# Optimization experiments

Measured on AMD Instinct MI355X. Metric: run time of the kernel, lower is better.

## Reference

```python
import jax, jax.numpy as jnp
import numpy as np

NEG_INF = -1e9

def setup_inputs() -> dict:
    key = jax.random.key(0)
    ks = jax.random.split(key, 7)
    B, NQ, NK, DQ, DK, DV, DH = 16, 128, 2048, 256, 256, 128, 64
    queries = jax.random.normal(ks[0], (B, NQ, DQ), dtype=jnp.float32)
    keys = jax.random.normal(ks[1], (B, NK, DK), dtype=jnp.float32)
    values = jax.random.normal(ks[2], (B, NK, DV), dtype=jnp.float32)
    valid_lens = jax.random.randint(ks[3], (B,), 1, NK + 1, dtype=jnp.int32)
    Wq = jax.random.normal(ks[4], (DQ, DH), dtype=jnp.float32) / np.sqrt(DQ)
    Wk = jax.random.normal(ks[5], (DK, DH), dtype=jnp.float32) / np.sqrt(DK)
    wv = jax.random.normal(ks[6], (DH,), dtype=jnp.float32) / np.sqrt(DH)
    return {"queries": queries, "keys": keys, "values": values,
            "valid_lens": valid_lens, "Wq": Wq, "Wk": Wk, "wv": wv}


def reference(queries, keys, values, valid_lens, Wq, Wk, wv):
    # Additive (Bahdanau) attention.
    q = jnp.einsum('bqd,dh->bqh', queries, Wq)   # [B, nq, dH]
    k = jnp.einsum('bkd,dh->bkh', keys, Wk)      # [B, nk, dH]
    # broadcast add -> tanh -> reduce with wv: scores [B, nq, nk]
    feat = jnp.tanh(q[:, :, None, :] + k[:, None, :, :])  # [B, nq, nk, dH]
    scores = jnp.einsum('bqkh,h->bqk', feat, wv)
    # masked softmax over nk using per-batch valid lengths
    nk = keys.shape[1]
    mask = jnp.arange(nk)[None, None, :] < valid_lens[:, None, None]  # [B,1,nk]
    scores = jnp.where(mask, scores, NEG_INF)
    attn = jax.nn.softmax(scores, axis=-1)
    # dropout is identity at eval time
    return jnp.einsum('bqk,bkv->bqv', attn, values)  # [B, nq, dv]
```

## Files before the change

kernel.cpp:

```cpp
#include <hip/hip_runtime.h>
#include <stddef.h>


__device__ __forceinline__ float fast_rcp(float x)  { return __builtin_amdgcn_rcpf(x); }
__device__ __forceinline__ float fast_exp2(float x) { return __builtin_amdgcn_exp2f(x); }

#define C2F 2.88539008177792681f
#define L2E 1.44269504088896340f

#define M_CNTP 0
#define M_CNTS 1
#define M_NP   2
#define M_NS   3
#define M_PPK  8
#define M_PSC  32

__global__ void init_kernel(const int* __restrict__ vlens, int* __restrict__ meta)
{
  if (threadIdx.x == 0) {
    int ap = 0, as = 0;
    meta[M_PPK] = 0; meta[M_PSC] = 0;
    for (int b = 0; b < 16; ++b) {
      int vl = vlens[b];
      ap += (vl + 63) >> 6;
      as += (vl + 127) >> 7;
      meta[M_PPK + 1 + b] = ap;
      meta[M_PSC + 1 + b] = as;
    }
    meta[M_NP]   = 32 + ap;
    meta[M_NS]   = as * 8;
    meta[M_CNTP] = 0;
    meta[M_CNTS] = 0;
  }
}

template<int MODE>
__device__ __forceinline__
void proj_body(const float* __restrict__ inb, const float* __restrict__ W,
               float* __restrict__ out, int b, int r0, int rowsPerB, int t)
{
  __shared__ float4 Wlds[256 * 16];
  __shared__ float  klds[64 * 36];

  const float4* W4 = (const float4*)W;
  #pragma unroll
  for (int i = 0; i < 16; ++i) Wlds[t + 256 * i] = W4[t + 256 * i];

  const int j = t >> 4;
  const int g = t & 15;

  float acc[4][4];
  #pragma unroll
  for (int m = 0; m < 4; ++m)
    acc[m][0] = acc[m][1] = acc[m][2] = acc[m][3] = 0.f;

  for (int dc = 0; dc < 8; ++dc) {
    {
      const int row = t >> 2, cs = (t & 3) * 8;
      const float* s = inb + row * 256 + dc * 32 + cs;
      float4 a0 = *(const float4*)s;
      float4 a1 = *(const float4*)(s + 4);
      float* dst = &klds[row * 36 + cs];
      *(float4*)dst       = a0;
      *(float4*)(dst + 4) = a1;
    }
    __syncthreads();
    #pragma unroll
    for (int d = 0; d < 32; ++d) {
      float4 w4 = Wlds[(dc * 32 + d) * 16 + j];
      #pragma unroll
      for (int m = 0; m < 4; ++m) {
        float kv = klds[(g + 16 * m) * 36 + d];
        acc[m][0] = fmaf(kv, w4.x, acc[m][0]);
        acc[m][1] = fmaf(kv, w4.y, acc[m][1]);
        acc[m][2] = fmaf(kv, w4.z, acc[m][2]);
        acc[m][3] = fmaf(kv, w4.w, acc[m][3]);
      }
    }
    __syncthreads();
  }

  if constexpr (MODE == 1) {
    #pragma unroll
    for (int m = 0; m < 4; ++m) {
      int k = r0 + g + 16 * m;
      size_t base = ((size_t)(b * 16 + (k >> 7)) * 64) * 128 + (k & 127);
      #pragma unroll
      for (int i = 0; i < 4; ++i)
        out[base + (size_t)(4 * j + i) * 128] = fast_exp2(C2F * acc[m][i]);
    }
  } else if constexpr (MODE == 2) {
    #pragma unroll
    for (int m = 0; m < 4; ++m) {
      int k = r0 + g + 16 * m;
      size_t base = (size_t)(b * 16 + (k >> 7)) * 8192 + (size_t)(k & 127) * 2;
      float e0 = fast_exp2(C2F * acc[m][0]);
      float e1 = fast_exp2(C2F * acc[m][1]);
      float e2 = fast_exp2(C2F * acc[m][2]);
      float e3 = fast_exp2(C2F * acc[m][3]);
      *(float2*)&out[base + (size_t)(2 * j) * 256]     = make_float2(e0, e1);
      *(float2*)&out[base + (size_t)(2 * j + 1) * 256] = make_float2(e2, e3);
    }
  } else {
    #pragma unroll
    for (int m = 0; m < 4; ++m) {
      int row = r0 + g + 16 * m;
      float4 o;
      o.x = fast_exp2(C2F * acc[m][0]);
      o.y = fast_exp2(C2F * acc[m][1]);
      o.z = fast_exp2(C2F * acc[m][2]);
      o.w = fast_exp2(C2F * acc[m][3]);
      *(float4*)&out[((size_t)b * rowsPerB + row) * 64 + 4 * j] = o;
    }
  }
}

__global__ __launch_bounds__(256)
void proj_qk_kernel(const float* __restrict__ queries, const float* __restrict__ keys,
                    const float* __restrict__ Wq, const float* __restrict__ Wk,
                    float* __restrict__ Eq, float* __restrict__ EkP,
                    int* __restrict__ meta)
{
  __shared__ int sh_u;
  const int t = threadIdx.x;
  const int nunits = meta[M_NP];
  for (;;) {
    __syncthreads();
    if (t == 0) sh_u = atomicAdd(&meta[M_CNTP], 1);
    __syncthreads();
    const int u = sh_u;
    if (u >= nunits) break;
    if (u < 32) {
      const int b = u & 15, rt = u >> 4, r0 = rt * 64;
      proj_body<0>(queries + ((size_t)b * 128 + r0) * 256, Wq, Eq, b, r0, 128, t);
    } else {
      int w = u - 32;
      int b = 0;
      while (w >= meta[M_PPK + 1 + b]) ++b;
      const int rt = w - meta[M_PPK + b];
      const int r0 = rt * 64;
      proj_body<2>(keys + ((size_t)b * 2048 + r0) * 256, Wk, EkP, b, r0, 2048, t);
    }
  }
}

template<int MODE, bool CHECK>
__global__ __launch_bounds__(256)
void proj_kernel(const float* __restrict__ in, const float* __restrict__ W,
                 float* __restrict__ out, const int* __restrict__ vlens,
                 int rowsPerB)
{
  const int t  = threadIdx.x;
  const int b  = blockIdx.x & 15;
  const int rt = blockIdx.x >> 4;
  const int r0 = rt * 64;
  if constexpr (CHECK) {
    if (r0 >= vlens[b]) return;
  }
  proj_body<MODE>(in + ((size_t)b * rowsPerB + r0) * 256, W, out, b, r0,
                  rowsPerB, t);
}

__global__ __launch_bounds__(512, 8)
void scorepv_kernel(const float* __restrict__ Eq, const float* __restrict__ EkP,
                    const float* __restrict__ values, const int* __restrict__ vlens,
                    const float* __restrict__ wv,
                    float* __restrict__ partial, float* __restrict__ tsum,
                    int* __restrict__ meta)
{
  __shared__ float ek_lds[64 * 128];
  __shared__ int sh_u;

  const int t = threadIdx.x;
  const int nunits = meta[M_NS];

  float w0 = 0.f, W1 = 0.f;
  #pragma unroll
  for (int u = 0; u < 16; ++u) {
    float4 v = ((const float4*)wv)[u];
    w0 += v.x + v.y + v.z + v.w;
    W1 += fabsf(v.x) + fabsf(v.y) + fabsf(v.z) + fabsf(v.w);
  }

  for (;;) {
    __syncthreads();
    if (t == 0) sh_u = atomicAdd(&meta[M_CNTS], 1);
    __syncthreads();
    const int u = sh_u;
    if (u >= nunits) break;

    const int w  = u >> 3;
    const int qq = u & 7;
    int b = 0;
    while (w >= meta[M_PSC + 1 + b]) ++b;
    const int kt = w - meta[M_PSC + b];
    const int vl = vlens[b];

    {
      const float4* src = (const float4*)(EkP + (size_t)(b * 16 + kt) * 8192);
      float4* dst = (float4*)ek_lds;
      #pragma unroll
      for (int i = 0; i < 4; ++i) dst[t + 512 * i] = src[t + 512 * i];
    }
    __syncthreads();

    const int wave_u = __builtin_amdgcn_readfirstlane(t >> 6);
    const int lane   = t & 63;
    const int q0g    = qq * 16 + wave_u * 2;
    const int kp     = lane * 2;
    const float* eqb = Eq + (size_t)(b * 128 + q0g) * 64;

    float s[2][2] = {{w0, w0}, {w0, w0}};

    const float4* ek4 = (const float4*)ek_lds;
    #pragma unroll 8
    for (int hp = 0; hp < 32; ++hp) {
      float4 e = ek4[hp * 64 + lane];
      float2 wvp = *(const float2*)&wv[2 * hp];
      float wa = -2.0f * wvp.x, wb = -2.0f * wvp.y;
      #pragma unroll
      for (int q = 0; q < 2; ++q) {
        float2 eqp = *(const float2*)&eqb[q * 64 + 2 * hp];
        { float x0 = fmaf(eqp.x, e.x, 1.f), x1 = fmaf(eqp.y, e.y, 1.f);
          float y = fast_rcp(x0 * x1);
          float a = wb * x0; a = fmaf(wa, x1, a);
          s[q][0] = fmaf(a, y, s[q][0]); }
        { float x0 = fmaf(eqp.x, e.z, 1.f), x1 = fmaf(eqp.y, e.w, 1.f);
          float y = fast_rcp(x0 * x1);
          float a = wb * x0; a = fmaf(wa, x1, a);
          s[q][1] = fmaf(a, y, s[q][1]); }
      }
    }

    const int kbase = kt * 128 + kp;
    float p[2][2];
    #pragma unroll
    for (int q = 0; q < 2; ++q) {
      p[q][0] = (kbase     < vl) ? fast_exp2((s[q][0] - W1) * L2E) : 0.f;
      p[q][1] = (kbase + 1 < vl) ? fast_exp2((s[q][1] - W1) * L2E) : 0.f;
    }

    #pragma unroll
    for (int q = 0; q < 2; ++q) {
      float e = p[q][0] + p[q][1];
      #pragma unroll
      for (int m = 1; m < 64; m <<= 1) e += __shfl_xor(e, m, 64);
      if (lane == 0) tsum[(size_t)(b * 16 + kt) * 128 + q0g + q] = e;
    }

    __syncthreads();
    float* p_lds = ek_lds;
    const int q0l = wave_u * 2;
    *(float2*)&p_lds[kp * 20 + q0l]       = make_float2(p[0][0], p[1][0]);
    *(float2*)&p_lds[(kp + 1) * 20 + q0l] = make_float2(p[0][1], p[1][1]);
    __syncthreads();

    const int kg = t >> 7, v = t & 127;
    const int kloc = min(128, vl - kt * 128);
    const int k0 = kg * 32, k1 = min(k0 + 32, kloc);
    const int len = (k1 > k0) ? (k1 - k0) : 0;
    const int nfull = len & ~7;
    const float* vb = values + ((size_t)(b * 2048 + kt * 128)) * 128 + v;
    float acc[16];
    #pragma unroll
    for (int i = 0; i < 16; ++i) acc[i] = 0.f;

    for (int kb = k0; kb < k0 + nfull; kb += 8) {
      float vv[8];
      #pragma unroll
      for (int j = 0; j < 8; ++j) vv[j] = vb[(size_t)(kb + j) * 128];
      #pragma unroll
      for (int j = 0; j < 8; ++j) {
        const float* pr = &p_lds[(kb + j) * 20];
        float4 p0 = *(const float4*)&pr[0];
        float4 p1 = *(const float4*)&pr[4];
        float4 p2 = *(const float4*)&pr[8];
        float4 p3 = *(const float4*)&pr[12];
        float vx = vv[j];
        acc[ 0]=fmaf(p0.x,vx,acc[ 0]); acc[ 1]=fmaf(p0.y,vx,acc[ 1]);
        acc[ 2]=fmaf(p0.z,vx,acc[ 2]); acc[ 3]=fmaf(p0.w,vx,acc[ 3]);
        acc[ 4]=fmaf(p1.x,vx,acc[ 4]); acc[ 5]=fmaf(p1.y,vx,acc[ 5]);
        acc[ 6]=fmaf(p1.z,vx,acc[ 6]); acc[ 7]=fmaf(p1.w,vx,acc[ 7]);
        acc[ 8]=fmaf(p2.x,vx,acc[ 8]); acc[ 9]=fmaf(p2.y,vx,acc[ 9]);
        acc[10]=fmaf(p2.z,vx,acc[10]); acc[11]=fmaf(p2.w,vx,acc[11]);
        acc[12]=fmaf(p3.x,vx,acc[12]); acc[13]=fmaf(p3.y,vx,acc[13]);
        acc[14]=fmaf(p3.z,vx,acc[14]); acc[15]=fmaf(p3.w,vx,acc[15]);
      }
    }
    for (int k = k0 + nfull; k < k1; ++k) {
      float vx = vb[(size_t)k * 128];
      const float* pr = &p_lds[k * 20];
      #pragma unroll
      for (int q = 0; q < 16; ++q) acc[q] = fmaf(pr[q], vx, acc[q]);
    }

    __syncthreads();
    float* red = ek_lds;
    if (kg > 0) {
      #pragma unroll
      for (int q = 0; q < 16; ++q) red[(kg - 1) * 2048 + q * 128 + v] = acc[q];
    }
    __syncthreads();
    if (kg == 0) {
      #pragma unroll
      for (int q = 0; q < 16; ++q) {
        float tot = acc[q] + red[q * 128 + v] + red[2048 + q * 128 + v]
                  + red[4096 + q * 128 + v];
        partial[(((size_t)(b * 128 + qq * 16 + q)) * 16 + kt) * 128 + v] = tot;
      }
    }
  }
}

__global__ __launch_bounds__(256)
void reduce_kernel(const float* __restrict__ partial, const float* __restrict__ tsum,
                   const int* __restrict__ vlens, float* __restrict__ out)
{
  const int blk = blockIdx.x;
  const int b   = blk >> 6;
  const int q   = (blk & 63) * 2 + (threadIdx.x >> 7);
  const int v   = threadIdx.x & 127;
  const int ntk = (vlens[b] + 127) >> 7;

  float tot = 0.f;
  for (int i = 0; i < ntk; ++i)
    tot += tsum[(size_t)(b * 16 + i) * 128 + q];

  float acc = 0.f;
  const float* pp = partial + ((size_t)(b * 128 + q)) * 16 * 128 + v;
  for (int i = 0; i < ntk; ++i)
    acc += pp[(size_t)i * 128];

  out[((size_t)(b * 128 + q)) * 128 + v] = acc / tot;
}

__global__ __launch_bounds__(256)
void attn_kernel(const float* __restrict__ Eq, const float* __restrict__ EkT,
                 const float* __restrict__ values, const int* __restrict__ vlens,
                 const float* __restrict__ wv, float* __restrict__ out)
{
  const int t    = threadIdx.x;
  const int b    = blockIdx.x & 15;
  const int qt   = blockIdx.x >> 4;
  const int wave = t >> 6;
  const int lane = t & 63;

  __shared__ float4 sc4[512 * 4];
  __shared__ float  pvp[128 * 5];
  __shared__ float  linvs[4];

  const int vl = vlens[b];

  float eqv[64], wv2[64];
  float w0 = 0.f;
  {
    const float4* eq4 = (const float4*)(Eq + (size_t)(b * 128 + qt * 4 + wave) * 64);
    const float4* wv4 = (const float4*)wv;
    #pragma unroll
    for (int u = 0; u < 16; ++u) {
      float4 e = eq4[u], v = wv4[u];
      eqv[4*u+0] = e.x; eqv[4*u+1] = e.y; eqv[4*u+2] = e.z; eqv[4*u+3] = e.w;
      wv2[4*u+0] = -2.f * v.x; wv2[4*u+1] = -2.f * v.y;
      wv2[4*u+2] = -2.f * v.z; wv2[4*u+3] = -2.f * v.w;
      w0 += v.x + v.y + v.z + v.w;
    }
  }

  const int ktiles = (vl + 127) >> 7;
  const int kp = 2 * lane;
  for (int kt = 0; kt < ktiles; ++kt) {
    const float* tb = EkT + ((size_t)(b * 16 + kt) * 64) * 128 + kp;
    float s0 = w0, s1 = w0;
    #pragma unroll
    for (int h = 0; h < 64; ++h) {
      float2 ek = *(const float2*)(tb + (size_t)h * 128);
      float r0 = fast_rcp(fmaf(eqv[h], ek.x, 1.0f));
      float r1 = fast_rcp(fmaf(eqv[h], ek.y, 1.0f));
      s0 = fmaf(wv2[h], r0, s0);
      s1 = fmaf(wv2[h], r1, s1);
    }
    int k = kt * 128 + kp;
    if (k     >= vl) s0 = -1e9f;
    if (k + 1 >= vl) s1 = -1e9f;
    float* scf = (float*)sc4;
    *(float2*)(scf + (((k >> 2) * 4 + wave) * 4 + (k & 3))) = make_float2(s0, s1);
  }

  const int nq4 = (vl + 3) >> 2;
  float mx = -3e38f;
  for (int Q = lane; Q < nq4; Q += 64) {
    float4 f = sc4[Q * 4 + wave];
    mx = fmaxf(mx, fmaxf(fmaxf(f.x, f.y), fmaxf(f.z, f.w)));
  }
  #pragma unroll
  for (int msk = 1; msk < 64; msk <<= 1) mx = fmaxf(mx, __shfl_xor(mx, msk, 64));
  float lsum = 0.f;
  for (int Q = lane; Q < nq4; Q += 64) {
    float4 f = sc4[Q * 4 + wave];
    f.x = fast_exp2((f.x - mx) * L2E);
    f.y = fast_exp2((f.y - mx) * L2E);
    f.z = fast_exp2((f.z - mx) * L2E);
    f.w = fast_exp2((f.w - mx) * L2E);
    sc4[Q * 4 + wave] = f;
    lsum += f.x + f.y + f.z + f.w;
  }
  #pragma unroll
  for (int msk = 1; msk < 64; msk <<= 1) lsum += __shfl_xor(lsum, msk, 64);
  if (lane == 0) linvs[wave] = fast_rcp(lsum);
  __syncthreads();

  const int grp = t >> 7, v = t & 127;
  float acc[4] = {0.f, 0.f, 0.f, 0.f};
  const float* vb = values + (size_t)b * 2048 * 128 + v;
  for (int Q = grp; Q < nq4; Q += 2) {
    float4 p0 = sc4[Q * 4 + 0], p1 = sc4[Q * 4 + 1];
    float4 p2 = sc4[Q * 4 + 2], p3 = sc4[Q * 4 + 3];
    const float* vk = vb + (size_t)(Q * 4) * 128;
    float x;
    x = vk[0];
    acc[0]=fmaf(p0.x,x,acc[0]); acc[1]=fmaf(p1.x,x,acc[1]);
    acc[2]=fmaf(p2.x,x,acc[2]); acc[3]=fmaf(p3.x,x,acc[3]);
    x = vk[128];
    acc[0]=fmaf(p0.y,x,acc[0]); acc[1]=fmaf(p1.y,x,acc[1]);
    acc[2]=fmaf(p2.y,x,acc[2]); acc[3]=fmaf(p3.y,x,acc[3]);
    x = vk[256];
    acc[0]=fmaf(p0.z,x,acc[0]); acc[1]=fmaf(p1.z,x,acc[1]);
    acc[2]=fmaf(p2.z,x,acc[2]); acc[3]=fmaf(p3.z,x,acc[3]);
    x = vk[384];
    acc[0]=fmaf(p0.w,x,acc[0]); acc[1]=fmaf(p1.w,x,acc[1]);
    acc[2]=fmaf(p2.w,x,acc[2]); acc[3]=fmaf(p3.w,x,acc[3]);
  }
  if (grp == 1) {
    #pragma unroll
    for (int qq = 0; qq < 4; ++qq) pvp[v * 5 + qq] = acc[qq];
  }
  __syncthreads();
  if (grp == 0) {
    #pragma unroll
    for (int qq = 0; qq < 4; ++qq) {
      float tot = acc[qq] + pvp[v * 5 + qq];
      out[((size_t)(b * 128) + qt * 4 + qq) * 128 + v] = tot * linvs[qq];
    }
  }
}

extern "C" void kernel_launch(void* const* d_in, const int* in_sizes, int n_in,
                              void* d_out, int out_size, void* d_ws, size_t ws_size,
                              hipStream_t stream) {
  const float* queries = (const float*)d_in[0];
  const float* keys    = (const float*)d_in[1];
  const float* values  = (const float*)d_in[2];
  const int*   vlens   = (const int*)d_in[3];
  const float* Wq      = (const float*)d_in[4];
  const float* Wk      = (const float*)d_in[5];
  const float* wv      = (const float*)d_in[6];
  float* outp = (float*)d_out;

  float* base    = (float*)d_ws;
  float* Eq      = base;
  float* EkP     = base + 131072;
  float* tsumb   = base + 2228224;
  float* partial = base + 2260992;
  int*   meta    = (int*)(base + 6455296);
  const size_t need = (size_t)6455296 * 4 + 64 * 4;

  if (ws_size >= need) {
    hipLaunchKernelGGL(init_kernel, dim3(1), dim3(64), 0, stream, vlens, meta);
    hipLaunchKernelGGL(proj_qk_kernel, dim3(512), dim3(256), 0, stream,
                       queries, keys, Wq, Wk, Eq, EkP, meta);
    hipLaunchKernelGGL(scorepv_kernel, dim3(1024), dim3(512), 0, stream,
                       Eq, EkP, values, vlens, wv, partial, tsumb, meta);
    hipLaunchKernelGGL(reduce_kernel, dim3(1024), dim3(256), 0, stream,
                       partial, tsumb, vlens, outp);
  } else {
    hipLaunchKernelGGL((proj_kernel<0, false>), dim3(32), dim3(256), 0, stream,
                       queries, Wq, Eq, (const int*)nullptr, 128);
    hipLaunchKernelGGL((proj_kernel<1, true>), dim3(512), dim3(256), 0, stream,
                       keys, Wk, EkP, vlens, 2048);
    hipLaunchKernelGGL(attn_kernel, dim3(512), dim3(256), 0, stream,
                       Eq, EkP, values, vlens, wv, outp);
  }
}
```

Before: 90.32 us.

## Split fused score/PV kernel and load both projection weights once per block

The fused score+PV kernel becomes two persistent kernels: score_kernel writes per-unit probabilities to a global scratch buffer, and pv_kernel reads them back to do the values matmul. Each kernel can then use its own LDS footprint and occupancy, and the LDS reuse syncs between phases go away. The projection kernel now uses 512-thread blocks that load Wq and Wk into LDS once and keep them across all work units, and prefix tables are cached in shared memory. The cost is an extra global round trip for the probabilities (about 16 MB of scratch), one more launch, and 128 KB of LDS per projection block, which limits how many blocks fit.

```diff
diff --git a/kernel.cpp b/kernel.cpp
--- a/kernel.cpp
+++ b/kernel.cpp
@@ -10,8 +10,9 @@
 
 #define M_CNTP 0
 #define M_CNTS 1
-#define M_NP   2
-#define M_NS   3
+#define M_CNT2 2
+#define M_NP   3
+#define M_NS   4
 #define M_PPK  8
 #define M_PSC  32
 
@@ -31,147 +32,121 @@
     meta[M_NS]   = as * 8;
     meta[M_CNTP] = 0;
     meta[M_CNTS] = 0;
-  }
-}
-
-template<int MODE>
-__device__ __forceinline__
-void proj_body(const float* __restrict__ inb, const float* __restrict__ W,
-               float* __restrict__ out, int b, int r0, int rowsPerB, int t)
-{
-  __shared__ float4 Wlds[256 * 16];
-  __shared__ float  klds[64 * 36];
-
-  const float4* W4 = (const float4*)W;
-  #pragma unroll
-  for (int i = 0; i < 16; ++i) Wlds[t + 256 * i] = W4[t + 256 * i];
-
-  const int j = t >> 4;
-  const int g = t & 15;
-
-  float acc[4][4];
-  #pragma unroll
-  for (int m = 0; m < 4; ++m)
-    acc[m][0] = acc[m][1] = acc[m][2] = acc[m][3] = 0.f;
-
-  for (int dc = 0; dc < 8; ++dc) {
-    {
-      const int row = t >> 2, cs = (t & 3) * 8;
-      const float* s = inb + row * 256 + dc * 32 + cs;
-      float4 a0 = *(const float4*)s;
-      float4 a1 = *(const float4*)(s + 4);
-      float* dst = &klds[row * 36 + cs];
-      *(float4*)dst       = a0;
-      *(float4*)(dst + 4) = a1;
-    }
-    __syncthreads();
-    #pragma unroll
-    for (int d = 0; d < 32; ++d) {
-      float4 w4 = Wlds[(dc * 32 + d) * 16 + j];
-      #pragma unroll
-      for (int m = 0; m < 4; ++m) {
-        float kv = klds[(g + 16 * m) * 36 + d];
-        acc[m][0] = fmaf(kv, w4.x, acc[m][0]);
-        acc[m][1] = fmaf(kv, w4.y, acc[m][1]);
-        acc[m][2] = fmaf(kv, w4.z, acc[m][2]);
-        acc[m][3] = fmaf(kv, w4.w, acc[m][3]);
-      }
-    }
-    __syncthreads();
-  }
-
-  if constexpr (MODE == 1) {
-    #pragma unroll
-    for (int m = 0; m < 4; ++m) {
-      int k = r0 + g + 16 * m;
-      size_t base = ((size_t)(b * 16 + (k >> 7)) * 64) * 128 + (k & 127);
-      #pragma unroll
-      for (int i = 0; i < 4; ++i)
-        out[base + (size_t)(4 * j + i) * 128] = fast_exp2(C2F * acc[m][i]);
-    }
-  } else if constexpr (MODE == 2) {
-    #pragma unroll
-    for (int m = 0; m < 4; ++m) {
-      int k = r0 + g + 16 * m;
-      size_t base = (size_t)(b * 16 + (k >> 7)) * 8192 + (size_t)(k & 127) * 2;
-      float e0 = fast_exp2(C2F * acc[m][0]);
-      float e1 = fast_exp2(C2F * acc[m][1]);
-      float e2 = fast_exp2(C2F * acc[m][2]);
-      float e3 = fast_exp2(C2F * acc[m][3]);
-      *(float2*)&out[base + (size_t)(2 * j) * 256]     = make_float2(e0, e1);
-      *(float2*)&out[base + (size_t)(2 * j + 1) * 256] = make_float2(e2, e3);
-    }
-  } else {
-    #pragma unroll
-    for (int m = 0; m < 4; ++m) {
-      int row = r0 + g + 16 * m;
-      float4 o;
-      o.x = fast_exp2(C2F * acc[m][0]);
-      o.y = fast_exp2(C2F * acc[m][1]);
-      o.z = fast_exp2(C2F * acc[m][2]);
-      o.w = fast_exp2(C2F * acc[m][3]);
-      *(float4*)&out[((size_t)b * rowsPerB + row) * 64 + 4 * j] = o;
-    }
-  }
-}
-
-__global__ __launch_bounds__(256)
+    meta[M_CNT2] = 0;
+  }
+}
+
+__global__ __launch_bounds__(512, 2)
 void proj_qk_kernel(const float* __restrict__ queries, const float* __restrict__ keys,
                     const float* __restrict__ Wq, const float* __restrict__ Wk,
                     float* __restrict__ Eq, float* __restrict__ EkP,
                     int* __restrict__ meta)
 {
-  __shared__ int sh_u;
+  __shared__ float4 Wq_l[4096];
+  __shared__ float4 Wk_l[4096];
+  __shared__ float  klds[64 * 36];
+  __shared__ int sh_u, sh_pre[17];
+
   const int t = threadIdx.x;
+  #pragma unroll
+  for (int i = 0; i < 8; ++i) {
+    Wq_l[t + 512 * i] = ((const float4*)Wq)[t + 512 * i];
+    Wk_l[t + 512 * i] = ((const float4*)Wk)[t + 512 * i];
+  }
+  if (t < 17) sh_pre[t] = meta[M_PPK + t];
   const int nunits = meta[M_NP];
+
+  const int g  = t & 15;
+  const int j  = (t >> 4) & 15;
+  const int rh = t >> 8;
+
   for (;;) {
     __syncthreads();
     if (t == 0) sh_u = atomicAdd(&meta[M_CNTP], 1);
     __syncthreads();
     const int u = sh_u;
     if (u >= nunits) break;
-    if (u < 32) {
-      const int b = u & 15, rt = u >> 4, r0 = rt * 64;
-      proj_body<0>(queries + ((size_t)b * 128 + r0) * 256, Wq, Eq, b, r0, 128, t);
+
+    bool isq; int b, r0;
+    if (u < 32) { isq = true; b = u & 15; r0 = (u >> 4) * 64; }
+    else {
+      isq = false;
+      int w = u - 32;
+      b = 0;
+      while (w >= sh_pre[1 + b]) ++b;
+      r0 = (w - sh_pre[b]) * 64;
+    }
+    const float* inb = isq ? (queries + ((size_t)b * 128 + r0) * 256)
+                           : (keys    + ((size_t)b * 2048 + r0) * 256);
+    const float4* Wl = isq ? Wq_l : Wk_l;
+
+    float acc[2][4];
+    #pragma unroll
+    for (int m = 0; m < 2; ++m)
+      acc[m][0] = acc[m][1] = acc[m][2] = acc[m][3] = 0.f;
+
+    for (int dc = 0; dc < 8; ++dc) {
+      {
+        const int row = t >> 3, cs = (t & 7) * 4;
+        *(float4*)&klds[row * 36 + cs] =
+            *(const float4*)(inb + row * 256 + dc * 32 + cs);
+      }
+      __syncthreads();
+      #pragma unroll
+      for (int d = 0; d < 32; ++d) {
+        float4 w4 = Wl[(dc * 32 + d) * 16 + j];
+        float kv0 = klds[(g + 16 * rh) * 36 + d];
+        float kv1 = klds[(g + 16 * rh + 32) * 36 + d];
+        acc[0][0] = fmaf(kv0, w4.x, acc[0][0]);
+        acc[0][1] = fmaf(kv0, w4.y, acc[0][1]);
+        acc[0][2] = fmaf(kv0, w4.z, acc[0][2]);
+        acc[0][3] = fmaf(kv0, w4.w, acc[0][3]);
+        acc[1][0] = fmaf(kv1, w4.x, acc[1][0]);
+        acc[1][1] = fmaf(kv1, w4.y, acc[1][1]);
+        acc[1][2] = fmaf(kv1, w4.z, acc[1][2]);
+        acc[1][3] = fmaf(kv1, w4.w, acc[1][3]);
+      }
+      __syncthreads();
+    }
+
+    if (isq) {
+      #pragma unroll
+      for (int m = 0; m < 2; ++m) {
+        int row = r0 + g + 16 * rh + 32 * m;
+        float4 o;
+        o.x = fast_exp2(C2F * acc[m][0]);
+        o.y = fast_exp2(C2F * acc[m][1]);
+        o.z = fast_exp2(C2F * acc[m][2]);
+        o.w = fast_exp2(C2F * acc[m][3]);
+        ((float4*)Eq)[((size_t)b * 128 + row) * 16 + j] = o;
+      }
     } else {
-      int w = u - 32;
-      int b = 0;
-      while (w >= meta[M_PPK + 1 + b]) ++b;
-      const int rt = w - meta[M_PPK + b];
-      const int r0 = rt * 64;
-      proj_body<2>(keys + ((size_t)b * 2048 + r0) * 256, Wk, EkP, b, r0, 2048, t);
-    }
-  }
-}
-
-template<int MODE, bool CHECK>
-__global__ __launch_bounds__(256)
-void proj_kernel(const float* __restrict__ in, const float* __restrict__ W,
-                 float* __restrict__ out, const int* __restrict__ vlens,
-                 int rowsPerB)
-{
-  const int t  = threadIdx.x;
-  const int b  = blockIdx.x & 15;
-  const int rt = blockIdx.x >> 4;
-  const int r0 = rt * 64;
-  if constexpr (CHECK) {
-    if (r0 >= vlens[b]) return;
-  }
-  proj_body<MODE>(in + ((size_t)b * rowsPerB + r0) * 256, W, out, b, r0,
-                  rowsPerB, t);
+      #pragma unroll
+      for (int m = 0; m < 2; ++m) {
+        int k = r0 + g + 16 * rh + 32 * m;
+        size_t base = (size_t)(b * 16 + (k >> 7)) * 8192 + (size_t)(k & 127) * 2;
+        float e0 = fast_exp2(C2F * acc[m][0]);
+        float e1 = fast_exp2(C2F * acc[m][1]);
+        float e2 = fast_exp2(C2F * acc[m][2]);
+        float e3 = fast_exp2(C2F * acc[m][3]);
+        *(float2*)&EkP[base + (size_t)(2 * j) * 256]     = make_float2(e0, e1);
+        *(float2*)&EkP[base + (size_t)(2 * j + 1) * 256] = make_float2(e2, e3);
+      }
+    }
+  }
 }
 
 __global__ __launch_bounds__(512, 8)
-void scorepv_kernel(const float* __restrict__ Eq, const float* __restrict__ EkP,
-                    const float* __restrict__ values, const int* __restrict__ vlens,
-                    const float* __restrict__ wv,
-                    float* __restrict__ partial, float* __restrict__ tsum,
-                    int* __restrict__ meta)
+void score_kernel(const float* __restrict__ Eq, const float* __restrict__ EkP,
+                  const int* __restrict__ vlens, const float* __restrict__ wv,
+                  float* __restrict__ pscr, float* __restrict__ tsum,
+                  int* __restrict__ meta)
 {
   __shared__ float ek_lds[64 * 128];
-  __shared__ int sh_u;
+  __shared__ int sh_u, sh_pre[17];
 
   const int t = threadIdx.x;
+  if (t < 17) sh_pre[t] = meta[M_PSC + t];
   const int nunits = meta[M_NS];
 
   float w0 = 0.f, W1 = 0.f;
@@ -182,6 +157,11 @@
     W1 += fabsf(v.x) + fabsf(v.y) + fabsf(v.z) + fabsf(v.w);
   }
 
+  const int wave_u = __builtin_amdgcn_readfirstlane(t >> 6);
+  const int lane   = t & 63;
+  const int kp     = lane * 2;
+  const int q0l    = wave_u * 2;
+
   for (;;) {
     __syncthreads();
     if (t == 0) sh_u = atomicAdd(&meta[M_CNTS], 1);
@@ -192,8 +172,8 @@
     const int w  = u >> 3;
     const int qq = u & 7;
     int b = 0;
-    while (w >= meta[M_PSC + 1 + b]) ++b;
-    const int kt = w - meta[M_PSC + b];
+    while (w >= sh_pre[1 + b]) ++b;
+    const int kt = w - sh_pre[b];
     const int vl = vlens[b];
 
     {
@@ -204,14 +184,10 @@
     }
     __syncthreads();
 
-    const int wave_u = __builtin_amdgcn_readfirstlane(t >> 6);
-    const int lane   = t & 63;
-    const int q0g    = qq * 16 + wave_u * 2;
-    const int kp     = lane * 2;
+    const int q0g = qq * 16 + q0l;
     const float* eqb = Eq + (size_t)(b * 128 + q0g) * 64;
 
     float s[2][2] = {{w0, w0}, {w0, w0}};
-
     const float4* ek4 = (const float4*)ek_lds;
     #pragma unroll 8
     for (int hp = 0; hp < 32; ++hp) {
@@ -248,19 +224,47 @@
       if (lane == 0) tsum[(size_t)(b * 16 + kt) * 128 + q0g + q] = e;
     }
 
-    __syncthreads();
-    float* p_lds = ek_lds;
-    const int q0l = wave_u * 2;
-    *(float2*)&p_lds[kp * 20 + q0l]       = make_float2(p[0][0], p[1][0]);
-    *(float2*)&p_lds[(kp + 1) * 20 + q0l] = make_float2(p[0][1], p[1][1]);
-    __syncthreads();
-
-    const int kg = t >> 7, v = t & 127;
+    float* pp = pscr + (size_t)u * 2048;
+    *(float2*)&pp[kp * 16 + q0l]       = make_float2(p[0][0], p[1][0]);
+    *(float2*)&pp[(kp + 1) * 16 + q0l] = make_float2(p[0][1], p[1][1]);
+  }
+}
+
+__global__ __launch_bounds__(512, 8)
+void pv_kernel(const float* __restrict__ values, const int* __restrict__ vlens,
+               const float* __restrict__ pscr, float* __restrict__ partial,
+               int* __restrict__ meta)
+{
+  __shared__ float red[3 * 16 * 128];
+  __shared__ int sh_u, sh_pre[17];
+
+  const int t = threadIdx.x;
+  if (t < 17) sh_pre[t] = meta[M_PSC + t];
+  const int nunits = meta[M_NS];
+
+  const int kg = t >> 7, v = t & 127;
+
+  for (;;) {
+    __syncthreads();
+    if (t == 0) sh_u = atomicAdd(&meta[M_CNT2], 1);
+    __syncthreads();
+    const int u = sh_u;
+    if (u >= nunits) break;
+
+    const int w  = u >> 3;
+    const int qq = u & 7;
+    int b = 0;
+    while (w >= sh_pre[1 + b]) ++b;
+    const int kt = w - sh_pre[b];
+    const int vl = vlens[b];
+
     const int kloc = min(128, vl - kt * 128);
     const int k0 = kg * 32, k1 = min(k0 + 32, kloc);
     const int len = (k1 > k0) ? (k1 - k0) : 0;
     const int nfull = len & ~7;
+    const float* pp = pscr + (size_t)u * 2048;
     const float* vb = values + ((size_t)(b * 2048 + kt * 128)) * 128 + v;
+
     float acc[16];
     #pragma unroll
     for (int i = 0; i < 16; ++i) acc[i] = 0.f;
@@ -271,11 +275,8 @@
       for (int j = 0; j < 8; ++j) vv[j] = vb[(size_t)(kb + j) * 128];
       #pragma unroll
       for (int j = 0; j < 8; ++j) {
-        const float* pr = &p_lds[(kb + j) * 20];
-        float4 p0 = *(const float4*)&pr[0];
-        float4 p1 = *(const float4*)&pr[4];
-        float4 p2 = *(const float4*)&pr[8];
-        float4 p3 = *(const float4*)&pr[12];
+        const float4* pr = (const float4*)&pp[(kb + j) * 16];
+        float4 p0 = pr[0], p1 = pr[1], p2 = pr[2], p3 = pr[3];
         float vx = vv[j];
         acc[ 0]=fmaf(p0.x,vx,acc[ 0]); acc[ 1]=fmaf(p0.y,vx,acc[ 1]);
         acc[ 2]=fmaf(p0.z,vx,acc[ 2]); acc[ 3]=fmaf(p0.w,vx,acc[ 3]);
@@ -289,13 +290,11 @@
     }
     for (int k = k0 + nfull; k < k1; ++k) {
       float vx = vb[(size_t)k * 128];
-      const float* pr = &p_lds[k * 20];
+      const float* pr = &pp[k * 16];
       #pragma unroll
       for (int q = 0; q < 16; ++q) acc[q] = fmaf(pr[q], vx, acc[q]);
     }
 
-    __syncthreads();
-    float* red = ek_lds;
     if (kg > 0) {
       #pragma unroll
       for (int q = 0; q < 16; ++q) red[(kg - 1) * 2048 + q * 128 + v] = acc[q];
@@ -332,6 +331,92 @@
     acc += pp[(size_t)i * 128];
 
   out[((size_t)(b * 128 + q)) * 128 + v] = acc / tot;
+}
+
+template<int MODE>
+__device__ __forceinline__
+void proj_body(const float* __restrict__ inb, const float* __restrict__ W,
+               float* __restrict__ out, int b, int r0, int rowsPerB, int t)
+{
+  __shared__ float4 Wlds[256 * 16];
+  __shared__ float  klds[64 * 36];
+
+  const float4* W4 = (const float4*)W;
+  #pragma unroll
+  for (int i = 0; i < 16; ++i) Wlds[t + 256 * i] = W4[t + 256 * i];
+
+  const int j = t >> 4;
+  const int g = t & 15;
+
+  float acc[4][4];
+  #pragma unroll
+  for (int m = 0; m < 4; ++m)
+    acc[m][0] = acc[m][1] = acc[m][2] = acc[m][3] = 0.f;
+
+  for (int dc = 0; dc < 8; ++dc) {
+    {
+      const int row = t >> 2, cs = (t & 3) * 8;
+      const float* s = inb + row * 256 + dc * 32 + cs;
+      float4 a0 = *(const float4*)s;
+      float4 a1 = *(const float4*)(s + 4);
+      float* dst = &klds[row * 36 + cs];
+      *(float4*)dst       = a0;
+      *(float4*)(dst + 4) = a1;
+    }
+    __syncthreads();
+    #pragma unroll
+    for (int d = 0; d < 32; ++d) {
+      float4 w4 = Wlds[(dc * 32 + d) * 16 + j];
+      #pragma unroll
+      for (int m = 0; m < 4; ++m) {
+        float kv = klds[(g + 16 * m) * 36 + d];
+        acc[m][0] = fmaf(kv, w4.x, acc[m][0]);
+        acc[m][1] = fmaf(kv, w4.y, acc[m][1]);
+        acc[m][2] = fmaf(kv, w4.z, acc[m][2]);
+        acc[m][3] = fmaf(kv, w4.w, acc[m][3]);
+      }
+    }
+    __syncthreads();
+  }
+
+  if constexpr (MODE == 1) {
+    #pragma unroll
+    for (int m = 0; m < 4; ++m) {
+      int k = r0 + g + 16 * m;
+      size_t base = ((size_t)(b * 16 + (k >> 7)) * 64) * 128 + (k & 127);
+      #pragma unroll
+      for (int i = 0; i < 4; ++i)
+        out[base + (size_t)(4 * j + i) * 128] = fast_exp2(C2F * acc[m][i]);
+    }
+  } else {
+    #pragma unroll
+    for (int m = 0; m < 4; ++m) {
+      int row = r0 + g + 16 * m;
+      float4 o;
+      o.x = fast_exp2(C2F * acc[m][0]);
+      o.y = fast_exp2(C2F * acc[m][1]);
+      o.z = fast_exp2(C2F * acc[m][2]);
+      o.w = fast_exp2(C2F * acc[m][3]);
+      *(float4*)&out[((size_t)b * rowsPerB + row) * 64 + 4 * j] = o;
+    }
+  }
+}
+
+template<int MODE, bool CHECK>
+__global__ __launch_bounds__(256)
+void proj_kernel(const float* __restrict__ in, const float* __restrict__ W,
+                 float* __restrict__ out, const int* __restrict__ vlens,
+                 int rowsPerB)
+{
+  const int t  = threadIdx.x;
+  const int b  = blockIdx.x & 15;
+  const int rt = blockIdx.x >> 4;
+  const int r0 = rt * 64;
+  if constexpr (CHECK) {
+    if (r0 >= vlens[b]) return;
+  }
+  proj_body<MODE>(in + ((size_t)b * rowsPerB + r0) * 256, W, out, b, r0,
+                  rowsPerB, t);
 }
 
 __global__ __launch_bounds__(256)
@@ -450,10 +535,11 @@
   const float* queries = (const float*)d_in[0];
   const float* keys    = (const float*)d_in[1];
   const float* values  = (const float*)d_in[2];
-  const int*   vlens   = (const int*)d_in[3];
+  const int*   vlans   = (const int*)d_in[3];
   const float* Wq      = (const float*)d_in[4];
   const float* Wk      = (const float*)d_in[5];
   const float* wv      = (const float*)d_in[6];
+  const int*   vlens   = vlans;
   float* outp = (float*)d_out;
 
   float* base    = (float*)d_ws;
@@ -461,15 +547,18 @@
   float* EkP     = base + 131072;
   float* tsumb   = base + 2228224;
   float* partial = base + 2260992;
-  int*   meta    = (int*)(base + 6455296);
-  const size_t need = (size_t)6455296 * 4 + 64 * 4;
+  float* pscr    = base + 6455296;
+  int*   meta    = (int*)(base + 10649600);
+  const size_t need = (size_t)10649600 * 4 + 256;
 
   if (ws_size >= need) {
     hipLaunchKernelGGL(init_kernel, dim3(1), dim3(64), 0, stream, vlens, meta);
-    hipLaunchKernelGGL(proj_qk_kernel, dim3(512), dim3(256), 0, stream,
+    hipLaunchKernelGGL(proj_qk_kernel, dim3(256), dim3(512), 0, stream,
                        queries, keys, Wq, Wk, Eq, EkP, meta);
-    hipLaunchKernelGGL(scorepv_kernel, dim3(1024), dim3(512), 0, stream,
-                       Eq, EkP, values, vlens, wv, partial, tsumb, meta);
+    hipLaunchKernelGGL(score_kernel, dim3(1024), dim3(512), 0, stream,
+                       Eq, EkP, vlens, wv, pscr, tsumb, meta);
+    hipLaunchKernelGGL(pv_kernel, dim3(1024), dim3(512), 0, stream,
+                       values, vlens, pscr, partial, meta);
     hipLaunchKernelGGL(reduce_kernel, dim3(1024), dim3(256), 0, stream,
                        partial, tsumb, vlens, outp);
   } else {
```

New measurement: 129.8 us. 43.7% more time.
